# Kernel optimization log

Measured on AMD Instinct MI355X. Metric: run time of the kernel, lower is better.

## Reference

```python
import jax, jax.numpy as jnp
import numpy as np


def setup_inputs() -> dict:
    key = jax.random.key(0)
    k1, k2, k3 = jax.random.split(key, 3)
    shape = (16, 128, 128, 64)  # [B, H, W, C]
    return {
        "query": jax.random.normal(k1, shape, dtype=jnp.float32),
        "keys": jax.random.normal(k2, shape, dtype=jnp.float32),
        "values": jax.random.normal(k3, shape, dtype=jnp.float32),
    }


def reference(query, keys, values):
    # Attention over channel dim C, feature dim = H*W.
    # scores[b, q, k] = sum_{h,w} Q[b,h,w,q] * K[b,h,w,k]
    scores = jnp.einsum("bhwq,bhwk->bqk", query, keys)
    attn = jax.nn.softmax(scores, axis=-1)  # softmax over keys k
    # out[b,h,w,q] = sum_k attn[b,q,k] * V[b,h,w,k]
    out = jnp.einsum("bqk,bhwk->bhwq", attn, values)
    return out
```

## Files before the change

### kernel.cpp

```cpp
#include <hip/hip_runtime.h>


#define S_SPLIT 32
#define CHUNK (16384 / S_SPLIT)
#define TILE_ROWS 32
#define NT (CHUNK / TILE_ROWS)

__global__ __launch_bounds__(256) void scores_kernel(
    const float* __restrict__ Q, const float* __restrict__ K,
    float* __restrict__ partial) {
  const int bs = blockIdx.x;
  const int b = bs / S_SPLIT;
  const int s = bs % S_SPLIT;
  const int tid = threadIdx.x;
  const int w = tid >> 6;
  const int l = tid & 63;
  const int q0 = (l >> 3) * 8;
  const int k0 = (l & 7) * 8;

  __shared__ union {
    struct { float4 q[2][512]; float4 k[2][512]; } t;
    float red[2][4096];
  } lds;

  float acc[8][8];
#pragma unroll
  for (int i = 0; i < 8; ++i)
#pragma unroll
    for (int j = 0; j < 8; ++j) acc[i][j] = 0.f;

  const float4* Qg = (const float4*)(Q + ((size_t)b * 16384 + (size_t)s * CHUNK) * 64);
  const float4* Kg = (const float4*)(K + ((size_t)b * 16384 + (size_t)s * CHUNK) * 64);

  lds.t.q[0][tid]       = Qg[tid];
  lds.t.q[0][tid + 256] = Qg[tid + 256];
  lds.t.k[0][tid]       = Kg[tid];
  lds.t.k[0][tid + 256] = Kg[tid + 256];

  for (int t = 0; t < NT; ++t) {
    __syncthreads();
    const int cb = t & 1;

    float4 pq0, pq1, pk0, pk1;
    if (t + 1 < NT) {
      pq0 = Qg[(t + 1) * 512 + tid];
      pq1 = Qg[(t + 1) * 512 + tid + 256];
      pk0 = Kg[(t + 1) * 512 + tid];
      pk1 = Kg[(t + 1) * 512 + tid + 256];
    }

#pragma unroll
    for (int i = 0; i < 8; ++i) {
      const int r = (i << 2) + w;
      float4 qa = lds.t.q[cb][r * 16 + (q0 >> 2)];
      float4 qb = lds.t.q[cb][r * 16 + (q0 >> 2) + 1];
      float4 ka = lds.t.k[cb][r * 16 + (k0 >> 2)];
      float4 kb = lds.t.k[cb][r * 16 + (k0 >> 2) + 1];
      float qv[8] = {qa.x, qa.y, qa.z, qa.w, qb.x, qb.y, qb.z, qb.w};
      float kv[8] = {ka.x, ka.y, ka.z, ka.w, kb.x, kb.y, kb.z, kb.w};
#pragma unroll
      for (int ii = 0; ii < 8; ++ii)
#pragma unroll
        for (int jj = 0; jj < 8; ++jj)
          acc[ii][jj] += qv[ii] * kv[jj];
    }

    if (t + 1 < NT) {
      const int nb = (t + 1) & 1;
      lds.t.q[nb][tid]       = pq0;
      lds.t.q[nb][tid + 256] = pq1;
      lds.t.k[nb][tid]       = pk0;
      lds.t.k[nb][tid + 256] = pk1;
    }
  }

  __syncthreads();
  if (w >= 2) {
    float4* dst = (float4*)lds.red[w - 2];
#pragma unroll
    for (int i = 0; i < 8; ++i) {
      dst[(q0 + i) * 16 + (k0 >> 2)]     = make_float4(acc[i][0], acc[i][1], acc[i][2], acc[i][3]);
      dst[(q0 + i) * 16 + (k0 >> 2) + 1] = make_float4(acc[i][4], acc[i][5], acc[i][6], acc[i][7]);
    }
  }
  __syncthreads();
  if (w < 2) {
    float4* dst = (float4*)lds.red[w];
#pragma unroll
    for (int i = 0; i < 8; ++i) {
      float4 u = dst[(q0 + i) * 16 + (k0 >> 2)];
      float4 v = dst[(q0 + i) * 16 + (k0 >> 2) + 1];
      dst[(q0 + i) * 16 + (k0 >> 2)]     = make_float4(u.x + acc[i][0], u.y + acc[i][1], u.z + acc[i][2], u.w + acc[i][3]);
      dst[(q0 + i) * 16 + (k0 >> 2) + 1] = make_float4(v.x + acc[i][4], v.y + acc[i][5], v.z + acc[i][6], v.w + acc[i][7]);
    }
  }
  __syncthreads();
  float4* p4 = (float4*)(partial + (size_t)bs * 4096);
  const float4* r0 = (const float4*)lds.red[0];
  const float4* r1 = (const float4*)lds.red[1];
#pragma unroll
  for (int c = 0; c < 4; ++c) {
    float4 x = r0[c * 256 + tid];
    float4 y = r1[c * 256 + tid];
    p4[c * 256 + tid] = make_float4(x.x + y.x, x.y + y.y, x.z + y.z, x.w + y.w);
  }
}

__global__ __launch_bounds__(64) void softmax_kernel(
    const float* __restrict__ partial, float* __restrict__ attn_t) {
  const int blk = blockIdx.x;
  const int b = blk >> 4;
  const int q0 = (blk & 15) * 4;
  const int lane = threadIdx.x;
  const int ql = lane >> 4;
  const int k4 = lane & 15;

  const float4* P = (const float4*)partial;
  float4 v = make_float4(0.f, 0.f, 0.f, 0.f);
  for (int s = 0; s < S_SPLIT; ++s) {
    float4 t = P[((size_t)(b * S_SPLIT + s) * 64 + q0 + ql) * 16 + k4];
    v.x += t.x; v.y += t.y; v.z += t.z; v.w += t.w;
  }

  float m = fmaxf(fmaxf(v.x, v.y), fmaxf(v.z, v.w));
#pragma unroll
  for (int off = 8; off > 0; off >>= 1)
    m = fmaxf(m, __shfl_xor(m, off, 64));
  float4 e = make_float4(__expf(v.x - m), __expf(v.y - m), __expf(v.z - m), __expf(v.w - m));
  float sum = e.x + e.y + e.z + e.w;
#pragma unroll
  for (int off = 8; off > 0; off >>= 1)
    sum += __shfl_xor(sum, off, 64);
  const float inv = 1.f / sum;

  float* A = attn_t + (size_t)b * 4096;
  A[(4 * k4 + 0) * 64 + q0 + ql] = e.x * inv;
  A[(4 * k4 + 1) * 64 + q0 + ql] = e.y * inv;
  A[(4 * k4 + 2) * 64 + q0 + ql] = e.z * inv;
  A[(4 * k4 + 3) * 64 + q0 + ql] = e.w * inv;
}

__global__ __launch_bounds__(256) void out_kernel(
    const float* __restrict__ V, const float* __restrict__ attn_t,
    float* __restrict__ out) {
  const int blk = blockIdx.x;
  const int b = blk >> 7;
  const int tile = blk & 127;
  const int tid = threadIdx.x;
  const int g = tid >> 4;
  const int qg = tid & 15;

  __shared__ float4 Vl[128 * 17];
  __shared__ float4 Al[64 * 16];

  const float4* Vg = (const float4*)(V + ((size_t)b * 16384 + (size_t)tile * 128) * 64);
#pragma unroll
  for (int u = 0; u < 8; ++u) {
    const int idx = u * 256 + tid;
    Vl[(idx >> 4) * 17 + (idx & 15)] = Vg[idx];
  }
  const float4* Ag = (const float4*)(attn_t + (size_t)b * 4096);
#pragma unroll
  for (int u = 0; u < 4; ++u)
    Al[u * 256 + tid] = Ag[u * 256 + tid];
  __syncthreads();

  float acc[8][4];
#pragma unroll
  for (int i = 0; i < 8; ++i)
#pragma unroll
    for (int j = 0; j < 4; ++j) acc[i][j] = 0.f;

  for (int k4 = 0; k4 < 16; ++k4) {
    const float4 a0 = Al[(4 * k4 + 0) * 16 + qg];
    const float4 a1 = Al[(4 * k4 + 1) * 16 + qg];
    const float4 a2 = Al[(4 * k4 + 2) * 16 + qg];
    const float4 a3 = Al[(4 * k4 + 3) * 16 + qg];
#pragma unroll
    for (int i = 0; i < 8; ++i) {
      const float4 v = Vl[(i * 16 + g) * 17 + k4];
      acc[i][0] += v.x * a0.x + v.y * a1.x + v.z * a2.x + v.w * a3.x;
      acc[i][1] += v.x * a0.y + v.y * a1.y + v.z * a2.y + v.w * a3.y;
      acc[i][2] += v.x * a0.z + v.y * a1.z + v.z * a2.z + v.w * a3.z;
      acc[i][3] += v.x * a0.w + v.y * a1.w + v.z * a2.w + v.w * a3.w;
    }
  }

  float4* og = (float4*)(out + ((size_t)b * 16384 + (size_t)tile * 128) * 64);
#pragma unroll
  for (int i = 0; i < 8; ++i) {
    const int row = i * 16 + g;
    og[row * 16 + qg] = make_float4(acc[i][0], acc[i][1], acc[i][2], acc[i][3]);
  }
}

extern "C" void kernel_launch(void* const* d_in, const int* in_sizes, int n_in,
                              void* d_out, int out_size, void* d_ws, size_t ws_size,
                              hipStream_t stream) {
  const float* Q = (const float*)d_in[0];
  const float* K = (const float*)d_in[1];
  const float* V = (const float*)d_in[2];
  float* out = (float*)d_out;

  float* partial = (float*)d_ws;
  float* attn_t = partial + (size_t)16 * S_SPLIT * 4096;

  scores_kernel<<<16 * S_SPLIT, 256, 0, stream>>>(Q, K, partial);
  softmax_kernel<<<16 * 16, 64, 0, stream>>>(partial, attn_t);
  out_kernel<<<16 * 128, 256, 0, stream>>>(V, attn_t, out);
}
```

Measured before the change: 227.3 us.

## Load Q/K/V directly from global into registers, drop LDS staging, raise split to 64

The scores kernel no longer stages Q/K tiles in LDS. Each wave reads its own rows straight from global memory into registers with a one-step register prefetch. The out kernel likewise reads V directly from global with register double-buffering instead of a padded LDS tile. The split over the spatial dimension grows from 32 to 64 when the workspace allows, which adds blocks but also doubles the partial buffer the softmax has to reduce. The aim is to remove LDS traffic and barriers, at the cost of strided global loads with less coalescing.

```diff
diff --git a/kernel.cpp b/kernel.cpp
--- a/kernel.cpp
+++ b/kernel.cpp
@@ -1,27 +1,22 @@
 #include <hip/hip_runtime.h>
 
 
-#define S_SPLIT 32
-#define CHUNK (16384 / S_SPLIT)
-#define TILE_ROWS 32
-#define NT (CHUNK / TILE_ROWS)
-
+template <int SPLIT>
 __global__ __launch_bounds__(256) void scores_kernel(
     const float* __restrict__ Q, const float* __restrict__ K,
     float* __restrict__ partial) {
+  constexpr int CH = 16384 / SPLIT;
+  constexpr int NI = CH / 4;
   const int bs = blockIdx.x;
-  const int b = bs / S_SPLIT;
-  const int s = bs % S_SPLIT;
+  const int b = bs / SPLIT;
+  const int s = bs % SPLIT;
   const int tid = threadIdx.x;
   const int w = tid >> 6;
   const int l = tid & 63;
   const int q0 = (l >> 3) * 8;
   const int k0 = (l & 7) * 8;
 
-  __shared__ union {
-    struct { float4 q[2][512]; float4 k[2][512]; } t;
-    float red[2][4096];
-  } lds;
+  __shared__ float red[2][4096];
 
   float acc[8][8];
 #pragma unroll
@@ -29,54 +24,38 @@
 #pragma unroll
     for (int j = 0; j < 8; ++j) acc[i][j] = 0.f;
 
-  const float4* Qg = (const float4*)(Q + ((size_t)b * 16384 + (size_t)s * CHUNK) * 64);
-  const float4* Kg = (const float4*)(K + ((size_t)b * 16384 + (size_t)s * CHUNK) * 64);
-
-  lds.t.q[0][tid]       = Qg[tid];
-  lds.t.q[0][tid + 256] = Qg[tid + 256];
-  lds.t.k[0][tid]       = Kg[tid];
-  lds.t.k[0][tid + 256] = Kg[tid + 256];
-
-  for (int t = 0; t < NT; ++t) {
-    __syncthreads();
-    const int cb = t & 1;
-
-    float4 pq0, pq1, pk0, pk1;
-    if (t + 1 < NT) {
-      pq0 = Qg[(t + 1) * 512 + tid];
-      pq1 = Qg[(t + 1) * 512 + tid + 256];
-      pk0 = Kg[(t + 1) * 512 + tid];
-      pk1 = Kg[(t + 1) * 512 + tid + 256];
-    }
-
-#pragma unroll
-    for (int i = 0; i < 8; ++i) {
-      const int r = (i << 2) + w;
-      float4 qa = lds.t.q[cb][r * 16 + (q0 >> 2)];
-      float4 qb = lds.t.q[cb][r * 16 + (q0 >> 2) + 1];
-      float4 ka = lds.t.k[cb][r * 16 + (k0 >> 2)];
-      float4 kb = lds.t.k[cb][r * 16 + (k0 >> 2) + 1];
-      float qv[8] = {qa.x, qa.y, qa.z, qa.w, qb.x, qb.y, qb.z, qb.w};
-      float kv[8] = {ka.x, ka.y, ka.z, ka.w, kb.x, kb.y, kb.z, kb.w};
-#pragma unroll
-      for (int ii = 0; ii < 8; ++ii)
-#pragma unroll
-        for (int jj = 0; jj < 8; ++jj)
-          acc[ii][jj] += qv[ii] * kv[jj];
-    }
-
-    if (t + 1 < NT) {
-      const int nb = (t + 1) & 1;
-      lds.t.q[nb][tid]       = pq0;
-      lds.t.q[nb][tid + 256] = pq1;
-      lds.t.k[nb][tid]       = pk0;
-      lds.t.k[nb][tid + 256] = pk1;
-    }
+  const float4* Qg = (const float4*)(Q + ((size_t)b * 16384 + (size_t)s * CH) * 64);
+  const float4* Kg = (const float4*)(K + ((size_t)b * 16384 + (size_t)s * CH) * 64);
+
+  int r = w;
+  float4 qa = Qg[r * 16 + (q0 >> 2)];
+  float4 qb = Qg[r * 16 + (q0 >> 2) + 1];
+  float4 ka = Kg[r * 16 + (k0 >> 2)];
+  float4 kb = Kg[r * 16 + (k0 >> 2) + 1];
+
+  for (int it = 0; it < NI; ++it) {
+    float4 nqa = qa, nqb = qb, nka = ka, nkb = kb;
+    const int rn = r + 4;
+    if (it + 1 < NI) {
+      nqa = Qg[rn * 16 + (q0 >> 2)];
+      nqb = Qg[rn * 16 + (q0 >> 2) + 1];
+      nka = Kg[rn * 16 + (k0 >> 2)];
+      nkb = Kg[rn * 16 + (k0 >> 2) + 1];
+    }
+    float qv[8] = {qa.x, qa.y, qa.z, qa.w, qb.x, qb.y, qb.z, qb.w};
+    float kv[8] = {ka.x, ka.y, ka.z, ka.w, kb.x, kb.y, kb.z, kb.w};
+#pragma unroll
+    for (int ii = 0; ii < 8; ++ii)
+#pragma unroll
+      for (int jj = 0; jj < 8; ++jj)
+        acc[ii][jj] += qv[ii] * kv[jj];
+    qa = nqa; qb = nqb; ka = nka; kb = nkb;
+    r = rn;
   }
 
   __syncthreads();
   if (w >= 2) {
-    float4* dst = (float4*)lds.red[w - 2];
+    float4* dst = (float4*)red[w - 2];
 #pragma unroll
     for (int i = 0; i < 8; ++i) {
       dst[(q0 + i) * 16 + (k0 >> 2)]     = make_float4(acc[i][0], acc[i][1], acc[i][2], acc[i][3]);
@@ -85,7 +64,7 @@
   }
   __syncthreads();
   if (w < 2) {
-    float4* dst = (float4*)lds.red[w];
+    float4* dst = (float4*)red[w];
 #pragma unroll
     for (int i = 0; i < 8; ++i) {
       float4 u = dst[(q0 + i) * 16 + (k0 >> 2)];
@@ -96,8 +75,8 @@
   }
   __syncthreads();
   float4* p4 = (float4*)(partial + (size_t)bs * 4096);
-  const float4* r0 = (const float4*)lds.red[0];
-  const float4* r1 = (const float4*)lds.red[1];
+  const float4* r0 = (const float4*)red[0];
+  const float4* r1 = (const float4*)red[1];
 #pragma unroll
   for (int c = 0; c < 4; ++c) {
     float4 x = r0[c * 256 + tid];
@@ -106,19 +85,20 @@
   }
 }
 
+template <int SPLIT>
 __global__ __launch_bounds__(64) void softmax_kernel(
     const float* __restrict__ partial, float* __restrict__ attn_t) {
   const int blk = blockIdx.x;
   const int b = blk >> 4;
   const int q0 = (blk & 15) * 4;
-  const int lane = threadIdx.x;
-  const int ql = lane >> 4;
-  const int k4 = lane & 15;
+  const int l = threadIdx.x;
+  const int ql = l >> 4;
+  const int k4 = l & 15;
 
   const float4* P = (const float4*)partial;
   float4 v = make_float4(0.f, 0.f, 0.f, 0.f);
-  for (int s = 0; s < S_SPLIT; ++s) {
-    float4 t = P[((size_t)(b * S_SPLIT + s) * 64 + q0 + ql) * 16 + k4];
+  for (int s = 0; s < SPLIT; ++s) {
+    float4 t = P[((size_t)(b * SPLIT + s) * 64 + q0 + ql) * 16 + k4];
     v.x += t.x; v.y += t.y; v.z += t.z; v.w += t.w;
   }
 
@@ -143,46 +123,53 @@
 __global__ __launch_bounds__(256) void out_kernel(
     const float* __restrict__ V, const float* __restrict__ attn_t,
     float* __restrict__ out) {
-  const int blk = blockIdx.x;
-  const int b = blk >> 7;
-  const int tile = blk & 127;
+  const int b = blockIdx.x >> 7;
+  const int tile = blockIdx.x & 127;
   const int tid = threadIdx.x;
   const int g = tid >> 4;
   const int qg = tid & 15;
 
-  __shared__ float4 Vl[128 * 17];
   __shared__ float4 Al[64 * 16];
 
-  const float4* Vg = (const float4*)(V + ((size_t)b * 16384 + (size_t)tile * 128) * 64);
-#pragma unroll
-  for (int u = 0; u < 8; ++u) {
-    const int idx = u * 256 + tid;
-    Vl[(idx >> 4) * 17 + (idx & 15)] = Vg[idx];
-  }
   const float4* Ag = (const float4*)(attn_t + (size_t)b * 4096);
 #pragma unroll
   for (int u = 0; u < 4; ++u)
     Al[u * 256 + tid] = Ag[u * 256 + tid];
   __syncthreads();
 
+  const float4* Vg = (const float4*)(V + ((size_t)b * 16384 + (size_t)tile * 128) * 64);
+
   float acc[8][4];
 #pragma unroll
   for (int i = 0; i < 8; ++i)
 #pragma unroll
     for (int j = 0; j < 4; ++j) acc[i][j] = 0.f;
 
+  float4 vc[8];
+#pragma unroll
+  for (int i = 0; i < 8; ++i) vc[i] = Vg[(i * 16 + g) * 16];
+
   for (int k4 = 0; k4 < 16; ++k4) {
+    float4 vn[8];
+    if (k4 < 15) {
+#pragma unroll
+      for (int i = 0; i < 8; ++i) vn[i] = Vg[(i * 16 + g) * 16 + k4 + 1];
+    }
     const float4 a0 = Al[(4 * k4 + 0) * 16 + qg];
     const float4 a1 = Al[(4 * k4 + 1) * 16 + qg];
     const float4 a2 = Al[(4 * k4 + 2) * 16 + qg];
     const float4 a3 = Al[(4 * k4 + 3) * 16 + qg];
 #pragma unroll
     for (int i = 0; i < 8; ++i) {
-      const float4 v = Vl[(i * 16 + g) * 17 + k4];
+      const float4 v = vc[i];
       acc[i][0] += v.x * a0.x + v.y * a1.x + v.z * a2.x + v.w * a3.x;
       acc[i][1] += v.x * a0.y + v.y * a1.y + v.z * a2.y + v.w * a3.y;
       acc[i][2] += v.x * a0.z + v.y * a1.z + v.z * a2.z + v.w * a3.z;
       acc[i][3] += v.x * a0.w + v.y * a1.w + v.z * a2.w + v.w * a3.w;
+    }
+    if (k4 < 15) {
+#pragma unroll
+      for (int i = 0; i < 8; ++i) vc[i] = vn[i];
     }
   }
 
@@ -202,10 +189,19 @@
   const float* V = (const float*)d_in[2];
   float* out = (float*)d_out;
 
-  float* partial = (float*)d_ws;
-  float* attn_t = partial + (size_t)16 * S_SPLIT * 4096;
-
-  scores_kernel<<<16 * S_SPLIT, 256, 0, stream>>>(Q, K, partial);
-  softmax_kernel<<<16 * 16, 64, 0, stream>>>(partial, attn_t);
-  out_kernel<<<16 * 128, 256, 0, stream>>>(V, attn_t, out);
-}
+  const size_t need64 = (size_t)16 * 64 * 4096 * 4 + (size_t)16 * 4096 * 4;
+
+  if (ws_size >= need64) {
+    float* partial = (float*)d_ws;
+    float* attn_t = partial + (size_t)16 * 64 * 4096;
+    scores_kernel<64><<<16 * 64, 256, 0, stream>>>(Q, K, partial);
+    softmax_kernel<64><<<16 * 16, 64, 0, stream>>>(partial, attn_t);
+    out_kernel<<<16 * 128, 256, 0, stream>>>(V, attn_t, out);
+  } else {
+    float* partial = (float*)d_ws;
+    float* attn_t = partial + (size_t)16 * 32 * 4096;
+    scores_kernel<32><<<16 * 32, 256, 0, stream>>>(Q, K, partial);
+    softmax_kernel<32><<<16 * 16, 64, 0, stream>>>(partial, attn_t);
+    out_kernel<<<16 * 128, 256, 0, stream>>>(V, attn_t, out);
+  }
+}
```

New measurement: 266.1 us. +17.1%, slower.
